# Kernel optimization log

Hardware: AMD Instinct MI355X
Metric: run time of the kernel (lower is better)

Reference implementation:

```python
import jax, jax.numpy as jnp
import numpy as np

NOPE, ROPE, LORA, VDIM = 128, 64, 512, 128
T, H, S = 1024, 16, 8192
NUM_CHUNKS = 4  # prefix chunks merged via online-softmax LSE combine
SCALING = (NOPE + ROPE) ** -0.5


def setup_inputs() -> dict:
    key = jax.random.key(0)
    k1, k2, k3, k4 = jax.random.split(key, 4)
    q = jax.random.normal(k1, (T, H, NOPE + ROPE), dtype=jnp.float32)
    kv_cache = jax.random.normal(k2, (S, LORA + ROPE), dtype=jnp.float32)  # latent KV cache [S, 576]
    w_kc = jax.random.normal(k3, (H, NOPE, LORA), dtype=jnp.float32) * (NOPE ** -0.5)
    w_vc = jax.random.normal(k4, (H, LORA, VDIM), dtype=jnp.float32) * (LORA ** -0.5)
    return {"q": q, "kv_cache": kv_cache, "w_kc": w_kc, "w_vc": w_vc}


def _chunk_attn(q_full, kv):
    # q_full: [T,H,576], kv chunk: [C,576] (MQA: single latent KV head)
    scores = jnp.einsum('thd,sd->ths', q_full, kv) * SCALING
    lse = jax.nn.logsumexp(scores, axis=-1)               # [T,H]
    p = jnp.exp(scores - lse[..., None])                  # [T,H,C]
    out = jnp.einsum('ths,sl->thl', p, kv[:, :LORA])      # value = latent kv_lora part
    return out, lse


def reference(q, kv_cache, w_kc, w_vc):
    # --- weight-absorbed query projection (forward_absorb) ---
    q_nope, q_pe = q[..., :NOPE], q[..., NOPE:]
    q_lora = jnp.einsum('thn,hnl->thl', q_nope, w_kc)     # bmm(q_nope^T, w_kc)
    q_full = jnp.concatenate([q_lora, q_pe], axis=-1)     # [T,H,576]

    # --- chunked MQA over latent cache with LSE merge (merge_state_v2) ---
    chunks = kv_cache.reshape(NUM_CHUNKS, S // NUM_CHUNKS, LORA + ROPE)
    acc_out, acc_lse = _chunk_attn(q_full, chunks[0])

    def merge(carry, kv):
        a_out, a_lse = carry
        o, lse = _chunk_attn(q_full, kv)
        new_lse = jnp.logaddexp(a_lse, lse)
        new_out = (a_out * jnp.exp(a_lse - new_lse)[..., None]
                   + o * jnp.exp(lse - new_lse)[..., None])
        return (new_out, new_lse), None

    (attn_out, _), _ = jax.lax.scan(merge, (acc_out, acc_lse), chunks[1:])

    # --- weight-absorbed value projection: bmm(attn^T, w_vc) ---
    out = jnp.einsum('thl,hlv->thv', attn_out, w_vc)      # [T,H,128]
    return out.reshape(T, H * VDIM)
```

## Files before the change

kernel.cpp:

```cpp
#include <hip/hip_runtime.h>
#include <stdint.h>
#include <stddef.h>

#define T_TOK 1024
#define NH    16
#define S_KV  8192
#define DQK   576
#define DV    512
#define NROWS (T_TOK*NH)
#define SCALING 0.072168783648703220563f
#define M_FIX 8.0f

#define SC 32
#define NT (S_KV/SC)
#define KV_CH (72*SC)
#define VT_CH (4*DV)

typedef __attribute__((ext_vector_type(8))) short bf16x8;
typedef __attribute__((ext_vector_type(4))) float f32x4;

__device__ __forceinline__ uint16_t f2bf(float f) {
  uint32_t u = __float_as_uint(f);
  u += 0x7FFFu + ((u >> 16) & 1u);
  return (uint16_t)(u >> 16);
}
__device__ __forceinline__ uint32_t pk2(float a, float b) {
  return (uint32_t)f2bf(a) | ((uint32_t)f2bf(b) << 16);
}
__device__ __forceinline__ void async16(void* lds, const void* g) {
  __builtin_amdgcn_global_load_lds((const __attribute__((address_space(1))) void*)g,
                                   (__attribute__((address_space(3))) void*)lds, 16, 0, 0);
}

__global__ void prep_qfull(const float* __restrict__ q, const float* __restrict__ w_kc,
                           uint16_t* __restrict__ q_full) {
  const int h = blockIdx.y, t0 = blockIdx.x * 32;
  const int tid = threadIdx.x;
  __shared__ float qn[32][128];
  #pragma unroll
  for (int r = 0; r < 4; ++r) {
    int idx4 = r * 256 + tid;
    int row = idx4 >> 5, c4 = (idx4 & 31) * 4;
    const float4 v = *(const float4*)(q + ((size_t)((t0 + row) * NH + h)) * 192 + c4);
    *(float4*)&qn[row][c4] = v;
  }
  __syncthreads();
  const int ty = tid >> 6, tx = tid & 63;
  float acc[8][8];
  #pragma unroll
  for (int i = 0; i < 8; ++i)
    #pragma unroll
    for (int j = 0; j < 8; ++j) acc[i][j] = 0.f;
  for (int n = 0; n < 128; ++n) {
    const float4 b0 = *(const float4*)(w_kc + ((size_t)(h * 128 + n)) * 512 + tx * 8);
    const float4 b1 = *(const float4*)(w_kc + ((size_t)(h * 128 + n)) * 512 + tx * 8 + 4);
    #pragma unroll
    for (int i = 0; i < 8; ++i) {
      const float a = qn[ty * 8 + i][n];
      acc[i][0] += a * b0.x; acc[i][1] += a * b0.y; acc[i][2] += a * b0.z; acc[i][3] += a * b0.w;
      acc[i][4] += a * b1.x; acc[i][5] += a * b1.y; acc[i][6] += a * b1.z; acc[i][7] += a * b1.w;
    }
  }
  #pragma unroll
  for (int i = 0; i < 8; ++i) {
    const size_t R = (size_t)(t0 + ty * 8 + i) * NH + h;
    uint4 o;
    o.x = pk2(acc[i][0]*SCALING, acc[i][1]*SCALING);
    o.y = pk2(acc[i][2]*SCALING, acc[i][3]*SCALING);
    o.z = pk2(acc[i][4]*SCALING, acc[i][5]*SCALING);
    o.w = pk2(acc[i][6]*SCALING, acc[i][7]*SCALING);
    *(uint4*)&q_full[R * DQK + tx * 8] = o;
  }
  {
    const int trow = tid >> 3, j0 = (tid & 7) * 8;
    const float* src = q + ((size_t)((t0 + trow) * NH + h)) * 192 + 128 + j0;
    const float4 a = *(const float4*)(src);
    const float4 b = *(const float4*)(src + 4);
    const size_t R = (size_t)(t0 + trow) * NH + h;
    uint4 o;
    o.x = pk2(a.x*SCALING, a.y*SCALING); o.y = pk2(a.z*SCALING, a.w*SCALING);
    o.z = pk2(b.x*SCALING, b.y*SCALING); o.w = pk2(b.z*SCALING, b.w*SCALING);
    *(uint4*)&q_full[R * DQK + 512 + j0] = o;
  }
}

__global__ void prep_kv(const float* __restrict__ kv, uint16_t* __restrict__ kv_t,
                        uint16_t* __restrict__ vt_t) {
  const int st = blockIdx.x, tid = threadIdx.x;
  uint16_t* kvo = kv_t + (size_t)st * (KV_CH * 8);
  #pragma unroll
  for (int r = 0; r < 9; ++r) {
    const int k = r * 256 + tid;
    const int dc = k >> 5, sl = k & 31;
    const float* src = kv + ((size_t)(st * SC + sl)) * DQK + dc * 8;
    const float4 a = *(const float4*)src;
    const float4 b = *(const float4*)(src + 4);
    uint4 o;
    o.x = pk2(a.x, a.y); o.y = pk2(a.z, a.w); o.z = pk2(b.x, b.y); o.w = pk2(b.z, b.w);
    *(uint4*)&kvo[(size_t)k * 8] = o;
  }
  uint16_t* vto = vt_t + (size_t)st * (VT_CH * 8);
  #pragma unroll
  for (int r = 0; r < 8; ++r) {
    const int k = r * 256 + tid;
    const int sc = k >> 9, v = k & 511;
    float val[8];
    #pragma unroll
    for (int e = 0; e < 8; ++e)
      val[e] = kv[((size_t)(st * SC + sc * 8 + e)) * DQK + v];
    uint4 o;
    o.x = pk2(val[0], val[1]); o.y = pk2(val[2], val[3]);
    o.z = pk2(val[4], val[5]); o.w = pk2(val[6], val[7]);
    *(uint4*)&vto[(size_t)k * 8] = o;
  }
}

__global__ void wvt_prep(const float* __restrict__ w_vc, uint16_t* __restrict__ wvt) {
  const int c = blockIdx.x * 256 + threadIdx.x;
  const int h = c >> 13, rem = c & 8191;
  const int lc = rem >> 7, v = rem & 127;
  const float* src = w_vc + ((size_t)h * 512 + lc * 8) * 128 + v;
  float val[8];
  #pragma unroll
  for (int e = 0; e < 8; ++e) val[e] = src[e * 128];
  uint4 o;
  o.x = pk2(val[0], val[1]); o.y = pk2(val[2], val[3]);
  o.z = pk2(val[4], val[5]); o.w = pk2(val[6], val[7]);
  *(uint4*)&wvt[(size_t)c * 8] = o;
}

__global__ __launch_bounds__(768, 3) void attn_kernel(
    const uint16_t* __restrict__ q_full, const uint16_t* __restrict__ kv_t,
    const uint16_t* __restrict__ vt_t, uint16_t* __restrict__ attn_o) {
  __shared__ short kv_lds[2][KV_CH * 8];
  __shared__ short P_lds[2][260 * 8];
  __shared__ float l_sh[64];

  const int tid = threadIdx.x;
  const int wv = tid >> 6, lane = tid & 63;
  const int cc = lane & 15, quad = lane >> 4;
  const int R0 = blockIdx.x * 64;

  if (wv < 4) {
    const int qh = wv & 1, sh = wv >> 1;
    bf16x8 qf[2][18];
    #pragma unroll
    for (int j = 0; j < 2; ++j) {
      const uint16_t* qrow = q_full + (size_t)(R0 + 32 * qh + 16 * j + cc) * DQK + quad * 8;
      #pragma unroll
      for (int kk = 0; kk < 18; ++kk)
        qf[j][kk] = *(const bf16x8*)(qrow + kk * 32);
    }
    const int sc0 = 2 * sh + (cc >> 3), e = cc & 7;
    const int qb0 = 32 * qh + quad * 4, qb1 = qb0 + 16;

    for (int st = 0; st <= NT; ++st) {
      __syncthreads();
      if (st < NT) {
        const short* kb = kv_lds[st & 1];
        f32x4 sa0 = {0.f,0.f,0.f,0.f}, sa1 = {0.f,0.f,0.f,0.f};
        #pragma unroll
        for (int kk = 0; kk < 18; ++kk) {
          const bf16x8 b0 = *(const bf16x8*)&kb[((kk * 4 + quad) * SC + sh * 16 + cc) * 8];
          sa0 = __builtin_amdgcn_mfma_f32_16x16x32_bf16(qf[0][kk], b0, sa0, 0, 0, 0);
          sa1 = __builtin_amdgcn_mfma_f32_16x16x32_bf16(qf[1][kk], b0, sa1, 0, 0, 0);
        }
        short* Pb = P_lds[st & 1];
        #pragma unroll
        for (int r = 0; r < 4; ++r) {
          Pb[(sc0 * 65 + qb0 + r) * 8 + e] = (short)f2bf(__expf(sa0[r] - M_FIX));
          Pb[(sc0 * 65 + qb1 + r) * 8 + e] = (short)f2bf(__expf(sa1[r] - M_FIX));
        }
      }
    }
    __syncthreads();
  } else {
    const int ci = wv - 4;
    f32x4 acc[4][4];
    #pragma unroll
    for (int a = 0; a < 4; ++a)
      #pragma unroll
      for (int b = 0; b < 4; ++b) acc[a][b] = (f32x4){0.f, 0.f, 0.f, 0.f};
    f32x4 accl[4];
    #pragma unroll
    for (int a = 0; a < 4; ++a) accl[a] = (f32x4){0.f, 0.f, 0.f, 0.f};
    bf16x8 ones;
    #pragma unroll
    for (int e2 = 0; e2 < 8; ++e2) ones[e2] = (short)0x3F80;

    {
      const uint16_t* kt = kv_t;
      #pragma unroll
      for (int r = 0; r < 5; ++r) {
        const int base = r * 512 + ci * 64;
        if (base < KV_CH)
          async16(&kv_lds[0][base * 8], kt + (size_t)(base + lane) * 8);
      }
    }

    for (int st = 0; st <= NT; ++st) {
      __syncthreads();
      bf16x8 vt4[4];
      if (st > 0) {
        const uint16_t* vtile = vt_t + (size_t)(st - 1) * (VT_CH * 8);
        #pragma unroll
        for (int vj = 0; vj < 4; ++vj)
          vt4[vj] = *(const bf16x8*)(vtile + (size_t)(quad * 512 + 64 * ci + 16 * vj + cc) * 8);
      }
      if (st + 1 < NT) {
        const uint16_t* kt = kv_t + (size_t)(st + 1) * (KV_CH * 8);
        short* dst = kv_lds[(st + 1) & 1];
        #pragma unroll
        for (int r = 0; r < 5; ++r) {
          const int base = r * 512 + ci * 64;
          if (base < KV_CH)
            async16(&dst[base * 8], kt + (size_t)(base + lane) * 8);
        }
      }
      if (st > 0) {
        const short* Pb = P_lds[(st - 1) & 1];
        bf16x8 af[4];
        #pragma unroll
        for (int q2 = 0; q2 < 4; ++q2)
          af[q2] = *(const bf16x8*)&Pb[(quad * 65 + 16 * q2 + cc) * 8];
        if (ci == 0) {
          #pragma unroll
          for (int q2 = 0; q2 < 4; ++q2)
            accl[q2] = __builtin_amdgcn_mfma_f32_16x16x32_bf16(af[q2], ones, accl[q2], 0, 0, 0);
        }
        #pragma unroll
        for (int q2 = 0; q2 < 4; ++q2)
          #pragma unroll
          for (int vj = 0; vj < 4; ++vj)
            acc[q2][vj] = __builtin_amdgcn_mfma_f32_16x16x32_bf16(af[q2], vt4[vj], acc[q2][vj], 0, 0, 0);
      }
    }
    if (ci == 0 && cc == 0) {
      #pragma unroll
      for (int q2 = 0; q2 < 4; ++q2)
        #pragma unroll
        for (int r = 0; r < 4; ++r)
          l_sh[16 * q2 + quad * 4 + r] = accl[q2][r];
    }
    __syncthreads();
    #pragma unroll
    for (int q2 = 0; q2 < 4; ++q2) {
      #pragma unroll
      for (int r = 0; r < 4; ++r) {
        const int row = 16 * q2 + quad * 4 + r;
        const float li = 1.0f / l_sh[row];
        #pragma unroll
        for (int vj = 0; vj < 4; ++vj)
          attn_o[(size_t)(R0 + row) * DV + 64 * ci + 16 * vj + cc] = f2bf(acc[q2][vj][r] * li);
      }
    }
  }
}

__global__ __launch_bounds__(256) void out_proj(const uint16_t* __restrict__ attn_o,
                                                const uint16_t* __restrict__ wvt,
                                                float* __restrict__ out) {
  const int h = blockIdx.y, t0 = blockIdx.x * 64;
  const int wv = threadIdx.x >> 6, lane = threadIdx.x & 63;
  const int cc = lane & 15, quad = lane >> 4;

  f32x4 acc[8];
  #pragma unroll
  for (int vj = 0; vj < 8; ++vj) acc[vj] = (f32x4){0.f, 0.f, 0.f, 0.f};

  const uint16_t* arow = attn_o + ((size_t)(t0 + wv * 16 + cc) * NH + h) * DV + quad * 8;
  const uint16_t* wb = wvt + (size_t)h * (64 * 128) * 8;
  #pragma unroll 4
  for (int kk = 0; kk < 16; ++kk) {
    const bf16x8 a = *(const bf16x8*)(arow + kk * 32);
    #pragma unroll
    for (int vj = 0; vj < 8; ++vj) {
      const bf16x8 b = *(const bf16x8*)(wb + (size_t)(((kk * 4 + quad) * 128) + 16 * vj + cc) * 8);
      acc[vj] = __builtin_amdgcn_mfma_f32_16x16x32_bf16(a, b, acc[vj], 0, 0, 0);
    }
  }
  #pragma unroll
  for (int vj = 0; vj < 8; ++vj)
    #pragma unroll
    for (int r = 0; r < 4; ++r)
      out[(size_t)(t0 + wv * 16 + quad * 4 + r) * (NH * 128) + h * 128 + 16 * vj + cc] = acc[vj][r];
}

extern "C" void kernel_launch(void* const* d_in, const int* in_sizes, int n_in,
                              void* d_out, int out_size, void* d_ws, size_t ws_size,
                              hipStream_t stream) {
  const float* q    = (const float*)d_in[0];
  const float* kv   = (const float*)d_in[1];
  const float* w_kc = (const float*)d_in[2];
  const float* w_vc = (const float*)d_in[3];
  float* out = (float*)d_out;

  char* ws = (char*)d_ws;
  const size_t SZ_QF = (size_t)NROWS * DQK * 2;
  const size_t SZ_KT = (size_t)NT * KV_CH * 16;
  const size_t SZ_VT = (size_t)NT * VT_CH * 16;
  const size_t SZ_AO = (size_t)NROWS * DV * 2;
  uint16_t* q_full = (uint16_t*)(ws);
  uint16_t* kv_t   = (uint16_t*)(ws + SZ_QF);
  uint16_t* vt_t   = (uint16_t*)(ws + SZ_QF + SZ_KT);
  uint16_t* attn_o = (uint16_t*)(ws + SZ_QF + SZ_KT + SZ_VT);
  uint16_t* wvt    = (uint16_t*)(ws + SZ_QF + SZ_KT + SZ_VT + SZ_AO);

  prep_qfull<<<dim3(32, 16), 256, 0, stream>>>(q, w_kc, q_full);
  prep_kv<<<NT, 256, 0, stream>>>(kv, kv_t, vt_t);
  wvt_prep<<<512, 256, 0, stream>>>(w_vc, wvt);
  attn_kernel<<<256, 768, 0, stream>>>(q_full, kv_t, vt_t, attn_o);
  out_proj<<<dim3(16, 16), 256, 0, stream>>>(attn_o, wvt, out);
}
```

Before: 417.6 us.

## Triple-buffer KV DMA with raw barriers and 32x32 MFMA for PV

Moves the KV LDS ring from two to three stages, prefetching two tiles ahead with explicit vmcnt waits and raw s_barrier instead of __syncthreads. The PV consumer waves switch from 16x16x32 to 32x32x16 MFMA and load V fragments one step ahead into registers. s_setprio is raised around the MFMA bursts. The aim is to hide global-load latency and cut barrier and instruction overhead. In exchange it uses more LDS, which may cut occupancy below the three-block launch bound, and the hand-counted vmcnt values are fragile.

```diff
diff --git a/kernel.cpp b/kernel.cpp
--- a/kernel.cpp
+++ b/kernel.cpp
@@ -18,6 +18,16 @@
 
 typedef __attribute__((ext_vector_type(8))) short bf16x8;
 typedef __attribute__((ext_vector_type(4))) float f32x4;
+typedef __attribute__((ext_vector_type(16))) float f32x16;
+
+#define RAW_BAR() do {                              \
+    __builtin_amdgcn_sched_barrier(0);              \
+    asm volatile("" ::: "memory");                  \
+    __builtin_amdgcn_s_barrier();                   \
+    asm volatile("" ::: "memory");                  \
+    __builtin_amdgcn_sched_barrier(0);              \
+  } while (0)
+#define VMW(N) asm volatile("s_waitcnt vmcnt(" #N ")" ::: "memory")
 
 __device__ __forceinline__ uint16_t f2bf(float f) {
   uint32_t u = __float_as_uint(f);
@@ -132,7 +142,7 @@
 __global__ __launch_bounds__(768, 3) void attn_kernel(
     const uint16_t* __restrict__ q_full, const uint16_t* __restrict__ kv_t,
     const uint16_t* __restrict__ vt_t, uint16_t* __restrict__ attn_o) {
-  __shared__ short kv_lds[2][KV_CH * 8];
+  __shared__ short kv_lds[3][KV_CH * 8];
   __shared__ short P_lds[2][260 * 8];
   __shared__ float l_sh[64];
 
@@ -154,106 +164,135 @@
     const int sc0 = 2 * sh + (cc >> 3), e = cc & 7;
     const int qb0 = 32 * qh + quad * 4, qb1 = qb0 + 16;
 
+    int buf3 = 0;
     for (int st = 0; st <= NT; ++st) {
-      __syncthreads();
+      RAW_BAR();
       if (st < NT) {
-        const short* kb = kv_lds[st & 1];
+        const short* kb = kv_lds[buf3];
+        buf3 = (buf3 == 2) ? 0 : buf3 + 1;
         f32x4 sa0 = {0.f,0.f,0.f,0.f}, sa1 = {0.f,0.f,0.f,0.f};
+        __builtin_amdgcn_s_setprio(1);
         #pragma unroll
         for (int kk = 0; kk < 18; ++kk) {
           const bf16x8 b0 = *(const bf16x8*)&kb[((kk * 4 + quad) * SC + sh * 16 + cc) * 8];
           sa0 = __builtin_amdgcn_mfma_f32_16x16x32_bf16(qf[0][kk], b0, sa0, 0, 0, 0);
           sa1 = __builtin_amdgcn_mfma_f32_16x16x32_bf16(qf[1][kk], b0, sa1, 0, 0, 0);
         }
-        short* Pb = P_lds[st & 1];
+        __builtin_amdgcn_s_setprio(0);
+        short* Pbw = P_lds[st & 1];
         #pragma unroll
         for (int r = 0; r < 4; ++r) {
-          Pb[(sc0 * 65 + qb0 + r) * 8 + e] = (short)f2bf(__expf(sa0[r] - M_FIX));
-          Pb[(sc0 * 65 + qb1 + r) * 8 + e] = (short)f2bf(__expf(sa1[r] - M_FIX));
-        }
+          Pbw[(sc0 * 65 + qb0 + r) * 8 + e] = (short)f2bf(__expf(sa0[r] - M_FIX));
+          Pbw[(sc0 * 65 + qb1 + r) * 8 + e] = (short)f2bf(__expf(sa1[r] - M_FIX));
+        }
+        asm volatile("s_waitcnt lgkmcnt(0)" ::: "memory");
+        __builtin_amdgcn_sched_barrier(0);
       }
     }
     __syncthreads();
   } else {
     const int ci = wv - 4;
-    f32x4 acc[4][4];
-    #pragma unroll
-    for (int a = 0; a < 4; ++a)
-      #pragma unroll
-      for (int b = 0; b < 4; ++b) acc[a][b] = (f32x4){0.f, 0.f, 0.f, 0.f};
-    f32x4 accl[4];
-    #pragma unroll
-    for (int a = 0; a < 4; ++a) accl[a] = (f32x4){0.f, 0.f, 0.f, 0.f};
+    const int hi = lane >> 5, l31 = lane & 31;
+    f32x16 acc[2][2];
+    #pragma unroll
+    for (int a = 0; a < 2; ++a)
+      #pragma unroll
+      for (int b = 0; b < 2; ++b)
+        #pragma unroll
+        for (int r = 0; r < 16; ++r) acc[a][b][r] = 0.f;
+    f32x16 accl[2];
+    #pragma unroll
+    for (int a = 0; a < 2; ++a)
+      #pragma unroll
+      for (int r = 0; r < 16; ++r) accl[a][r] = 0.f;
     bf16x8 ones;
     #pragma unroll
     for (int e2 = 0; e2 < 8; ++e2) ones[e2] = (short)0x3F80;
 
-    {
-      const uint16_t* kt = kv_t;
+    #pragma unroll
+    for (int t = 0; t < 2; ++t) {
+      const uint16_t* kt = kv_t + (size_t)t * (KV_CH * 8);
+      short* dst = kv_lds[t];
       #pragma unroll
       for (int r = 0; r < 5; ++r) {
         const int base = r * 512 + ci * 64;
-        if (base < KV_CH)
-          async16(&kv_lds[0][base * 8], kt + (size_t)(base + lane) * 8);
-      }
-    }
-
+        if (base < KV_CH) async16(&dst[base * 8], kt + (size_t)(base + lane) * 8);
+      }
+    }
+
+    bf16x8 vt_cur[2][2];
+    int dmabuf = 2;
     for (int st = 0; st <= NT; ++st) {
-      __syncthreads();
-      bf16x8 vt4[4];
+      if (st == 0)        { if (ci < 4) { VMW(5); } else { VMW(4); } }
+      else if (st <= 254) { if (ci < 4) { VMW(9); } else { VMW(8); } }
+      else if (st == 255) { VMW(4); }
+      RAW_BAR();
       if (st > 0) {
-        const uint16_t* vtile = vt_t + (size_t)(st - 1) * (VT_CH * 8);
-        #pragma unroll
-        for (int vj = 0; vj < 4; ++vj)
-          vt4[vj] = *(const bf16x8*)(vtile + (size_t)(quad * 512 + 64 * ci + 16 * vj + cc) * 8);
-      }
-      if (st + 1 < NT) {
-        const uint16_t* kt = kv_t + (size_t)(st + 1) * (KV_CH * 8);
-        short* dst = kv_lds[(st + 1) & 1];
+        const short* Pb = P_lds[(st - 1) & 1];
+        bf16x8 af[2][2];
+        #pragma unroll
+        for (int qb = 0; qb < 2; ++qb)
+          #pragma unroll
+          for (int kh = 0; kh < 2; ++kh)
+            af[qb][kh] = *(const bf16x8*)&Pb[((2 * kh + hi) * 65 + qb * 32 + l31) * 8];
+        __builtin_amdgcn_s_setprio(1);
+        #pragma unroll
+        for (int qb = 0; qb < 2; ++qb)
+          #pragma unroll
+          for (int kh = 0; kh < 2; ++kh)
+            #pragma unroll
+            for (int vb = 0; vb < 2; ++vb)
+              acc[qb][vb] = __builtin_amdgcn_mfma_f32_32x32x16_bf16(
+                  af[qb][kh], vt_cur[vb][kh], acc[qb][vb], 0, 0, 0);
+        if (ci == 0) {
+          #pragma unroll
+          for (int qb = 0; qb < 2; ++qb)
+            #pragma unroll
+            for (int kh = 0; kh < 2; ++kh)
+              accl[qb] = __builtin_amdgcn_mfma_f32_32x32x16_bf16(
+                  af[qb][kh], ones, accl[qb], 0, 0, 0);
+        }
+        __builtin_amdgcn_s_setprio(0);
+      }
+      if (st < NT) {
+        const uint16_t* vtile = vt_t + (size_t)st * (VT_CH * 8);
+        #pragma unroll
+        for (int vb = 0; vb < 2; ++vb)
+          #pragma unroll
+          for (int kh = 0; kh < 2; ++kh)
+            vt_cur[vb][kh] = *(const bf16x8*)(vtile +
+                (size_t)((2 * kh + hi) * 512 + 64 * ci + 32 * vb + l31) * 8);
+      }
+      if (st + 2 < NT) {
+        const uint16_t* kt = kv_t + (size_t)(st + 2) * (KV_CH * 8);
+        short* dst = kv_lds[dmabuf];
+        dmabuf = (dmabuf == 2) ? 0 : dmabuf + 1;
         #pragma unroll
         for (int r = 0; r < 5; ++r) {
           const int base = r * 512 + ci * 64;
-          if (base < KV_CH)
-            async16(&dst[base * 8], kt + (size_t)(base + lane) * 8);
-        }
-      }
-      if (st > 0) {
-        const short* Pb = P_lds[(st - 1) & 1];
-        bf16x8 af[4];
-        #pragma unroll
-        for (int q2 = 0; q2 < 4; ++q2)
-          af[q2] = *(const bf16x8*)&Pb[(quad * 65 + 16 * q2 + cc) * 8];
-        if (ci == 0) {
-          #pragma unroll
-          for (int q2 = 0; q2 < 4; ++q2)
-            accl[q2] = __builtin_amdgcn_mfma_f32_16x16x32_bf16(af[q2], ones, accl[q2], 0, 0, 0);
-        }
-        #pragma unroll
-        for (int q2 = 0; q2 < 4; ++q2)
-          #pragma unroll
-          for (int vj = 0; vj < 4; ++vj)
-            acc[q2][vj] = __builtin_amdgcn_mfma_f32_16x16x32_bf16(af[q2], vt4[vj], acc[q2][vj], 0, 0, 0);
-      }
-    }
-    if (ci == 0 && cc == 0) {
-      #pragma unroll
-      for (int q2 = 0; q2 < 4; ++q2)
-        #pragma unroll
-        for (int r = 0; r < 4; ++r)
-          l_sh[16 * q2 + quad * 4 + r] = accl[q2][r];
+          if (base < KV_CH) async16(&dst[base * 8], kt + (size_t)(base + lane) * 8);
+        }
+      }
+    }
+    if (ci == 0 && l31 == 0) {
+      #pragma unroll
+      for (int qb = 0; qb < 2; ++qb)
+        #pragma unroll
+        for (int r = 0; r < 16; ++r)
+          l_sh[32 * qb + (r & 3) + 8 * (r >> 2) + 4 * hi] = accl[qb][r];
     }
     __syncthreads();
     #pragma unroll
-    for (int q2 = 0; q2 < 4; ++q2) {
-      #pragma unroll
-      for (int r = 0; r < 4; ++r) {
-        const int row = 16 * q2 + quad * 4 + r;
-        const float li = 1.0f / l_sh[row];
-        #pragma unroll
-        for (int vj = 0; vj < 4; ++vj)
-          attn_o[(size_t)(R0 + row) * DV + 64 * ci + 16 * vj + cc] = f2bf(acc[q2][vj][r] * li);
-      }
-    }
+    for (int qb = 0; qb < 2; ++qb)
+      #pragma unroll
+      for (int vb = 0; vb < 2; ++vb)
+        #pragma unroll
+        for (int r = 0; r < 16; ++r) {
+          const int row = 32 * qb + (r & 3) + 8 * (r >> 2) + 4 * hi;
+          const float li = 1.0f / l_sh[row];
+          attn_o[(size_t)(R0 + row) * DV + 64 * ci + 32 * vb + l31] =
+              f2bf(acc[qb][vb][r] * li);
+        }
   }
 }
 
```

After: 451.0 us. +8.0%, slower.
